# Performance work log

Measured on AMD Instinct MI355X. Metric: run time of the kernel, lower is better.

Reference implementation:

```python
import jax, jax.numpy as jnp
import numpy as np

H = 64          # hidden_size / SINDy latent dim
DM = 128        # d_model (GRU input size)
FF = 128        # dim_feedforward
NL = 2          # num_sindy_layers
EPS = 1e-5      # LayerNorm eps (torch default)
TRI_I, TRI_J = np.triu_indices(H)          # poly_order=2 pairs, torch loop order (i<=j)
LIB = 1 + H + TRI_I.size                   # 2145


def layernorm(x, g, b):
    m = jnp.mean(x, axis=-1, keepdims=True)
    v = jnp.mean((x - m) ** 2, axis=-1, keepdims=True)
    return (x - m) * jax.lax.rsqrt(v + EPS) * g + b


def sindy_library(z):
    # z: (N, H) -> Theta: (N, 1 + H + H*(H+1)/2); same term ordering as torch loops
    ones = jnp.ones((z.shape[0], 1), z.dtype)
    quad = z[:, TRI_I] * z[:, TRI_J]
    return jnp.concatenate([ones, z, quad], axis=1)


def gru_layer(x, Wih, Whh, bih, bhh):
    # x: (B, S, in), Wih: (3H, in), Whh: (3H, H); torch GRU gate order r,z,n
    xp = jnp.einsum('bsi,gi->bsg', x, Wih) + bih  # (B,S,3H) precomputed input projections
    B = x.shape[0]

    def step(h, xpt):
        gh = h @ Whh.T + bhh
        r = jax.nn.sigmoid(xpt[:, :H] + gh[:, :H])
        z = jax.nn.sigmoid(xpt[:, H:2 * H] + gh[:, H:2 * H])
        n = jnp.tanh(xpt[:, 2 * H:] + r * gh[:, 2 * H:])
        h = (1.0 - z) * n + z * h
        return h, h

    h0 = jnp.zeros((B, H), x.dtype)
    _, ys = jax.lax.scan(step, h0, jnp.swapaxes(xp, 0, 1))  # scan over time
    return jnp.swapaxes(ys, 0, 1)  # (B, S, H)


def sindy_layer(src, coef, g1, b1n, W1, bf1, W2, bf2, g2, b2n):
    B, S, _ = src.shape
    theta = sindy_library(src.reshape(-1, H))          # (N, LIB)
    upd = (theta @ coef).reshape(B, S, H)              # (B, S, H)
    src = layernorm(src + upd, g1, b1n)                # dropout = identity (eval)
    ff = jax.nn.gelu(src @ W1.T + bf1, approximate=False) @ W2.T + bf2
    return layernorm(src + ff, g2, b2n)


def setup_inputs() -> dict:
    key = jax.random.key(0)
    ks = jax.random.split(key, 24)
    f = lambda k, sh, s=0.05: (jax.random.normal(k, sh, dtype=jnp.float32) * s)
    inp = {
        'x': jax.random.normal(ks[0], (32, 500, DM), dtype=jnp.float32),
        # GRU layer 0 (input DM) and layer 1 (input H)
        'Wih0': f(ks[1], (3 * H, DM)), 'Whh0': f(ks[2], (3 * H, H)),
        'bih0': f(ks[3], (3 * H,)), 'bhh0': f(ks[4], (3 * H,)),
        'Wih1': f(ks[5], (3 * H, H)), 'Whh1': f(ks[6], (3 * H, H)),
        'bih1': f(ks[7], (3 * H,)), 'bhh1': f(ks[8], (3 * H,)),
        # stacked params for NL=2 identical SINDy layers
        'coeffs': f(ks[9], (NL, LIB, H), 0.02),
        'ln1_g': jnp.ones((NL, H), jnp.float32), 'ln1_b': jnp.zeros((NL, H), jnp.float32),
        'W1': f(ks[10], (NL, FF, H)), 'b1': f(ks[11], (NL, FF)),
        'W2': f(ks[12], (NL, H, FF)), 'b2': f(ks[13], (NL, H)),
        'ln2_g': jnp.ones((NL, H), jnp.float32), 'ln2_b': jnp.zeros((NL, H), jnp.float32),
    }
    return inp


def reference(x, Wih0, Whh0, bih0, bhh0, Wih1, Whh1, bih1, bhh1,
              coeffs, ln1_g, ln1_b, W1, b1, W2, b2, ln2_g, ln2_b):
    h = gru_layer(x, Wih0, Whh0, bih0, bhh0)
    h = gru_layer(h, Wih1, Whh1, bih1, bhh1)
    for l in range(NL):
        h = sindy_layer(h, coeffs[l], ln1_g[l], ln1_b[l], W1[l], b1[l],
                        W2[l], b2[l], ln2_g[l], ln2_b[l])
    return h, h[:, -1, :]
```

## Files before the change

### kernel.cpp

```cpp
#include <hip/hip_runtime.h>
#include <hip/hip_bf16.h>
#include <math.h>

#define H 64
#define DM 128
#define GDIM 192
#define BSZ 32
#define SEQ 500
#define NROW (BSZ*SEQ)
#define LIBN 2145
#define FFD 128
#define NKC2 75
#define NGRP 300
#define CPK2 153600

typedef __attribute__((ext_vector_type(8))) short short8;
typedef __attribute__((ext_vector_type(4))) float f32x4;
typedef __attribute__((ext_vector_type(2))) float f32x2;
typedef __attribute__((ext_vector_type(4))) unsigned u32x4;

__device__ __forceinline__ float sigf(float x) {
    return 1.0f / (1.0f + __expf(-x));
}
__device__ __forceinline__ float tanhfast(float x) {
    x = fminf(fmaxf(x, -15.0f), 15.0f);
    float t = __expf(-2.0f * x);
    return (1.0f - t) / (1.0f + t);
}
__device__ __forceinline__ short bf16r(float f) {
    unsigned u = __float_as_uint(f);
    unsigned r = (u + 0x7fffu + ((u >> 16) & 1u)) >> 16;
    return (short)r;
}
__device__ __forceinline__ f32x2 pkfma(f32x2 a, f32x2 b, f32x2 c) {
    f32x2 d;
    asm("v_pk_fma_f32 %0, %1, %2, %3" : "=v"(d) : "v"(a), "v"(b), "v"(c));
    return d;
}

__device__ __forceinline__ void grp_decode(int g, int& a, int& b) {
    if (g < 8) { a = 64; b = g * 8; }
    else if (g == 8 || g >= 297) { a = 64; b = 64; }
    else {
        int G = g - 9, acc = 0;
        a = 0; b = 0;
        for (int i2 = 0; i2 < 64; i2++) {
            int cnt = 8 - (i2 >> 3);
            if (G < acc + cnt) { a = i2; b = ((i2 >> 3) + (G - acc)) * 8; break; }
            acc += cnt;
        }
    }
}

__global__ void pack_all(const float* __restrict__ wih0,
                         const float* __restrict__ coeffs,
                         const float* __restrict__ w1,
                         const float* __restrict__ w2,
                         float* __restrict__ wtp,
                         short* __restrict__ bfa) {
    int idx = blockIdx.x * 256 + threadIdx.x;
    if (idx < GDIM * DM) {
        int k = idx / GDIM;
        int g = idx - k * GDIM;
        wtp[idx] = wih0[g * DM + k];
        return;
    }
    int r = idx - GDIM * DM;
    int l = r / (CPK2 + 2 * 8192);
    int q = r % (CPK2 + 2 * 8192);
    if (q < CPK2) {
        const float* coef = coeffs + (size_t)l * LIBN * H;
        int j = q & 7, lane = (q >> 3) & 63, nt = (q >> 9) & 3, kc = q >> 11;
        int grp = kc * 4 + (lane >> 4);
        int row = -1;
        if (grp < 8) row = 1 + grp * 8 + j;
        else if (grp == 8) row = (j == 0) ? 0 : -1;
        else if (grp < 297) {
            int a, b;
            grp_decode(grp, a, b);
            int jdx = b + j;
            if (jdx >= a) row = 65 + a * 64 - (a * (a - 1)) / 2 + (jdx - a);
        }
        int c = nt * 16 + (lane & 15);
        bfa[(size_t)l * CPK2 + q] = (row >= 0) ? bf16r(coef[(size_t)row * H + c]) : (short)0;
        return;
    }
    int q2 = q - CPK2;
    if (q2 < 8192) {
        const float* w1l = w1 + (size_t)l * FFD * H;
        int j = q2 & 7, lane = (q2 >> 3) & 63, nt = (q2 >> 9) & 7, kc = q2 >> 12;
        int k = kc * 32 + ((lane >> 4) << 3) + j;
        int n = nt * 16 + (lane & 15);
        bfa[(size_t)2 * CPK2 + l * 8192 + q2] = bf16r(w1l[(size_t)n * H + k]);
        return;
    }
    int q3 = q2 - 8192;
    const float* w2l = w2 + (size_t)l * H * FFD;
    int j = q3 & 7, lane = (q3 >> 3) & 63, nt = (q3 >> 9) & 3, kc = q3 >> 11;
    int k = kc * 32 + ((lane >> 4) << 3) + j;
    int n = nt * 16 + (lane & 15);
    bfa[(size_t)2 * CPK2 + 2 * 8192 + l * 8192 + q3] = bf16r(w2l[(size_t)n * FFD + k]);
}

__global__ __launch_bounds__(256, 1) void xp0_gemm(const float* __restrict__ x,
                                                   const float* __restrict__ wt2,
                                                   const float* __restrict__ bih0,
                                                   float* __restrict__ xpT) {
    __shared__ __align__(16) float wlds[DM * GDIM];
    int tid = threadIdx.x;
    int wv = __builtin_amdgcn_readfirstlane(tid >> 6);
    int lane = tid & 63;

    for (int p = tid; p < DM * GDIM / 4; p += 256)
        ((f32x4*)wlds)[p] = ((const f32x4*)wt2)[p];

    int i = lane >> 2;
    int j = lane & 3;
    int rb = blockIdx.x * 64;
    int row0 = rb + 4 * i;

    f32x4 acc[3][4];
#pragma unroll
    for (int t = 0; t < 3; t++) {
        f32x4 bv = *(const f32x4*)(bih0 + 16 * (wv + 4 * t) + 4 * j);
#pragma unroll
        for (int ii = 0; ii < 4; ii++) acc[t][ii] = bv;
    }
    __syncthreads();

    const float* xr0 = x + (size_t)row0 * DM;
    for (int k4 = 0; k4 < 32; k4++) {
        f32x4 xr[4];
#pragma unroll
        for (int ii = 0; ii < 4; ii++)
            xr[ii] = *(const f32x4*)(xr0 + ii * DM + k4 * 4);
#pragma unroll
        for (int t = 0; t < 3; t++) {
            int cb = 16 * (wv + 4 * t);
#pragma unroll
            for (int e = 0; e < 4; e++) {
                f32x4 wvv = *(const f32x4*)&wlds[(k4 * 4 + e) * GDIM + cb + 4 * j];
#pragma unroll
                for (int ii = 0; ii < 4; ii++)
                    acc[t][ii] += wvv * xr[ii][e];
            }
        }
    }
    int bb = row0 / 500;
    int ss = row0 - bb * 500;
    float* base = xpT + ((size_t)(bb * 125 + (ss >> 2)) * GDIM) * 4;
#pragma unroll
    for (int t = 0; t < 3; t++) {
        int cb = 16 * (wv + 4 * t);
#pragma unroll
        for (int jj = 0; jj < 4; jj++) {
            int g = cb + 4 * j + jj;
            f32x4 v = { acc[t][0][jj], acc[t][1][jj], acc[t][2][jj], acc[t][3][jj] };
            *(f32x4*)(base + (size_t)g * 4) = v;
        }
    }
}

__global__ __launch_bounds__(768, 3) void gru_fused(const float* __restrict__ xpT,
                                                    const float* __restrict__ whh0,
                                                    const float* __restrict__ bhh0,
                                                    const float* __restrict__ wih1,
                                                    const float* __restrict__ bih1,
                                                    const float* __restrict__ whh1,
                                                    const float* __restrict__ bhh1,
                                                    float* __restrict__ hbuf) {
    int b = blockIdx.x;
    int tid = threadIdx.x;
    int wv = __builtin_amdgcn_readfirstlane(tid >> 6);
    int lane = tid & 63;
    int m = wv % 3;
    int q = wv / 3;
    int k0 = q * 16;

    __shared__ __align__(16) float h0s[H];
    __shared__ __align__(16) float h1s[H];
    __shared__ float part[3][4][GDIM];

    if (tid < H) { h0s[tid] = 0.0f; h1s[tid] = 0.0f; }

    const float* W = (m == 0) ? whh0 : (m == 1) ? wih1 : whh1;
    f32x2 wrp[8], wzp[8], wnp[8];
#pragma unroll
    for (int k4 = 0; k4 < 4; k4++) {
        f32x4 a = ((const f32x4*)(W + (size_t)lane * H + k0))[k4];
        f32x4 c = ((const f32x4*)(W + (size_t)(H + lane) * H + k0))[k4];
        f32x4 d = ((const f32x4*)(W + (size_t)(2 * H + lane) * H + k0))[k4];
        wrp[2*k4]   = __builtin_shufflevector(a, a, 0, 1);
        wrp[2*k4+1] = __builtin_shufflevector(a, a, 2, 3);
        wzp[2*k4]   = __builtin_shufflevector(c, c, 0, 1);
        wzp[2*k4+1] = __builtin_shufflevector(c, c, 2, 3);
        wnp[2*k4]   = __builtin_shufflevector(d, d, 0, 1);
        wnp[2*k4+1] = __builtin_shufflevector(d, d, 2, 3);
    }

    float b0r = 0, b0z = 0, b0n = 0;
    float b1ir = 0, b1iz = 0, b1in = 0, b1hr = 0, b1hz = 0, b1hn = 0;
    float hreg0 = 0.0f, hreg1 = 0.0f;
    float hb4[4] = {0.f, 0.f, 0.f, 0.f};
    f32x4 xc[4][3];
    const float* xpB = xpT + (size_t)b * 125 * GDIM * 4;

    if (wv == 0) {
        b0r = bhh0[lane]; b0z = bhh0[H + lane]; b0n = bhh0[2 * H + lane];
#pragma unroll
        for (int g3 = 0; g3 < 3; g3++) {
            xc[0][g3] = *(const f32x4*)(xpB + ((size_t)0 * GDIM + g3 * 64 + lane) * 4);
            xc[1][g3] = *(const f32x4*)(xpB + ((size_t)1 * GDIM + g3 * 64 + lane) * 4);
        }
    } else if (wv == 2) {
        b1ir = bih1[lane]; b1iz = bih1[H + lane]; b1in = bih1[2 * H + lane];
        b1hr = bhh1[lane]; b1hz = bhh1[H + lane]; b1hn = bhh1[2 * H + lane];
    }
    __syncthreads();

    auto loadch = [&](int c, int buf) {
        if (c < 125) {
#pragma unroll
            for (int g3 = 0; g3 < 3; g3++)
                xc[buf][g3] = *(const f32x4*)(xpB + ((size_t)c * GDIM + g3 * 64 + lane) * 4);
        }
    };

    auto step = [&](int s, int e, float xr, float xz, float xn) {
        const float* hv = (m == 2) ? h1s : h0s;
        f32x2 arp = {0.f, 0.f}, azp = {0.f, 0.f}, anp = {0.f, 0.f};
#pragma unroll
        for (int t4 = 0; t4 < 4; t4++) {
            f32x4 h4 = ((const f32x4*)(hv + k0))[t4];
            f32x2 hlo = __builtin_shufflevector(h4, h4, 0, 1);
            f32x2 hhi = __builtin_shufflevector(h4, h4, 2, 3);
            arp = pkfma(wrp[2*t4], hlo, arp);
            arp = pkfma(wrp[2*t4+1], hhi, arp);
            azp = pkfma(wzp[2*t4], hlo, azp);
            azp = pkfma(wzp[2*t4+1], hhi, azp);
            anp = pkfma(wnp[2*t4], hlo, anp);
            anp = pkfma(wnp[2*t4+1], hhi, anp);
        }
        part[m][q][lane] = arp[0] + arp[1];
        part[m][q][H + lane] = azp[0] + azp[1];
        part[m][q][2 * H + lane] = anp[0] + anp[1];
        __syncthreads();

        if (wv == 0) {
            if (s < SEQ) {
                float gr = b0r, gz = b0z, gn = b0n;
#pragma unroll
                for (int qq = 0; qq < 4; qq++) {
                    gr += part[0][qq][lane];
                    gz += part[0][qq][H + lane];
                    gn += part[0][qq][2 * H + lane];
                }
                float rg = sigf(xr + gr);
                float zg = sigf(xz + gz);
                float ng = tanhfast(xn + rg * gn);
                hreg0 = (1.0f - zg) * ng + zg * hreg0;
                h0s[lane] = hreg0;
            }
        } else if (wv == 2) {
            if (s >= 1) {
                float xr1 = b1ir, xz1 = b1iz, xn1 = b1in;
                float gr1 = b1hr, gz1 = b1hz, gn1 = b1hn;
#pragma unroll
                for (int qq = 0; qq < 4; qq++) {
                    xr1 += part[1][qq][lane];
                    xz1 += part[1][qq][H + lane];
                    xn1 += part[1][qq][2 * H + lane];
                    gr1 += part[2][qq][lane];
                    gz1 += part[2][qq][H + lane];
                    gn1 += part[2][qq][2 * H + lane];
                }
                float rg = sigf(xr1 + gr1);
                float zg = sigf(xz1 + gz1);
                float ng = tanhfast(xn1 + rg * gn1);
                hreg1 = (1.0f - zg) * ng + zg * hreg1;
                h1s[lane] = hreg1;
                hb4[(e + 3) & 3] = hreg1;
                if (e == 0) {
                    float* dst = hbuf + ((size_t)b * SEQ + (s - 4)) * H + lane;
#pragma unroll
                    for (int t = 0; t < 4; t++) dst[t * H] = hb4[t];
                }
            }
        }
        __syncthreads();
    };

    for (int scb = 0; scb < 31; scb++) {
#pragma unroll
        for (int sci = 0; sci < 4; sci++) {
            int sc = scb * 4 + sci;
            if (wv == 0 && (sci & 1) == 0) {
                loadch(sc + 2, (sci + 2) & 3);
                loadch(sc + 3, (sci + 3) & 3);
            }
            int s0 = sc * 4;
            step(s0 + 0, 0, xc[sci][0][0], xc[sci][1][0], xc[sci][2][0]);
            step(s0 + 1, 1, xc[sci][0][1], xc[sci][1][1], xc[sci][2][1]);
            step(s0 + 2, 2, xc[sci][0][2], xc[sci][1][2], xc[sci][2][2]);
            step(s0 + 3, 3, xc[sci][0][3], xc[sci][1][3], xc[sci][2][3]);
        }
    }
    {
        step(496, 0, xc[0][0][0], xc[0][1][0], xc[0][2][0]);
        step(497, 1, xc[0][0][1], xc[0][1][1], xc[0][2][1]);
        step(498, 2, xc[0][0][2], xc[0][1][2], xc[0][2][2]);
        step(499, 3, xc[0][0][3], xc[0][1][3], xc[0][2][3]);
    }
    step(500, 0, 0.0f, 0.0f, 0.0f);
}

__global__ __launch_bounds__(512) void sindy_fused(const float* __restrict__ hbuf_in,
                                                   const short* __restrict__ bfa,
                                                   const float* __restrict__ ln1g,
                                                   const float* __restrict__ ln1b,
                                                   const float* __restrict__ b1g,
                                                   const float* __restrict__ b2g,
                                                   const float* __restrict__ ln2g,
                                                   const float* __restrict__ ln2b,
                                                   float* __restrict__ out) {
    __shared__ float z[65 * 68];
    __shared__ float upd[64 * 68];
    __shared__ float ff[64 * 132];
    __shared__ unsigned kmap2[NGRP];
    __shared__ float bfs1[2][FFD], bfs2[2][H];
    __shared__ float g1s[2][H], b1s[2][H], g2s[2][H], b2s[2][H];

    int tid = threadIdx.x;
    int wv = __builtin_amdgcn_readfirstlane(tid >> 6);
    int lane = tid & 63;
    int row0 = blockIdx.x * 64;

    for (int idx = tid; idx < 64 * 16; idx += 512) {
        int r = idx >> 4, c4 = idx & 15;
        *(f32x4*)&z[r * 68 + c4 * 4] = *(const f32x4*)&hbuf_in[(size_t)(row0 + r) * H + c4 * 4];
    }
    for (int idx = tid; idx < 64 * 17; idx += 512)
        *(f32x4*)&upd[idx * 4] = (f32x4){0.f, 0.f, 0.f, 0.f};
    if (tid < 64) {
        z[tid * 68 + 64] = 1.0f; z[tid * 68 + 65] = 0.0f;
        z[tid * 68 + 66] = 0.0f; z[tid * 68 + 67] = 0.0f;
    }
    if (tid < 68) z[64 * 68 + tid] = 0.0f;
    if (tid < NGRP) {
        int a, b;
        grp_decode(tid, a, b);
        kmap2[tid] = ((unsigned)a << 16) | (unsigned)b;
    }
    if (tid < FFD) { bfs1[0][tid] = b1g[tid]; bfs1[1][tid] = b1g[FFD + tid]; }
    if (tid < H) {
        bfs2[0][tid] = b2g[tid];      bfs2[1][tid] = b2g[H + tid];
        g1s[0][tid] = ln1g[tid];      g1s[1][tid] = ln1g[H + tid];
        b1s[0][tid] = ln1b[tid];      b1s[1][tid] = ln1b[H + tid];
        g2s[0][tid] = ln2g[tid];      g2s[1][tid] = ln2g[H + tid];
        b2s[0][tid] = ln2b[tid];      b2s[1][tid] = ln2b[H + tid];
    }
    __syncthreads();

    int kj0 = ((lane >> 4) << 3);
    int m0 = (wv & 3) * 16;
    int m = m0 + (lane & 15);
    int rbase = m0 + ((lane >> 4) << 2);
    int cb16 = lane & 15;
    const float* zrow = &z[m * 68];
    int lrow = tid >> 3;
    int lk = (tid & 7) * 8;

#pragma unroll
    for (int l = 0; l < 2; l++) {
        const short* cpk = bfa + (size_t)l * CPK2;
        const short* w1p = bfa + (size_t)2 * CPK2 + l * 8192;
        const short* w2p = bfa + (size_t)2 * CPK2 + 2 * 8192 + l * 8192;

        {
            int p = wv >> 2;
            f32x4 acc[4] = {{0,0,0,0},{0,0,0,0},{0,0,0,0},{0,0,0,0}};
            for (int kc = p; kc < NKC2; kc += 2) {
                unsigned ab = kmap2[kc * 4 + (lane >> 4)];
                float za = zrow[ab >> 16];
                const float* zb = &zrow[ab & 0xffffu];
                f32x4 z0 = *(const f32x4*)zb;
                f32x4 z1 = *(const f32x4*)(zb + 4);
                short8 af;
                af[0] = bf16r(za * z0[0]);
                af[1] = bf16r(za * z0[1]);
                af[2] = bf16r(za * z0[2]);
                af[3] = bf16r(za * z0[3]);
                af[4] = bf16r(za * z1[0]);
                af[5] = bf16r(za * z1[1]);
                af[6] = bf16r(za * z1[2]);
                af[7] = bf16r(za * z1[3]);
                const short* cb = cpk + ((size_t)(kc * 4) * 64 + lane) * 8;
#pragma unroll
                for (int nt = 0; nt < 4; nt++) {
                    short8 bf = *(const short8*)(cb + (size_t)nt * 512);
                    acc[nt] = __builtin_amdgcn_mfma_f32_16x16x32_bf16(af, bf, acc[nt], 0, 0, 0);
                }
            }
#pragma unroll
            for (int nt = 0; nt < 4; nt++)
#pragma unroll
                for (int r = 0; r < 4; r++)
                    atomicAdd(&upd[(rbase + r) * 68 + nt * 16 + cb16], acc[nt][r]);
        }
        __syncthreads();

        {
            float v[8];
            float s1 = 0.0f;
#pragma unroll
            for (int i = 0; i < 8; i++) {
                v[i] = z[lrow * 68 + lk + i] + upd[lrow * 68 + lk + i];
                s1 += v[i];
            }
            s1 += __shfl_xor(s1, 1); s1 += __shfl_xor(s1, 2); s1 += __shfl_xor(s1, 4);
            float mn = s1 * (1.0f / 64.0f);
            float s2 = 0.0f;
#pragma unroll
            for (int i = 0; i < 8; i++) { float d = v[i] - mn; s2 += d * d; }
            s2 += __shfl_xor(s2, 1); s2 += __shfl_xor(s2, 2); s2 += __shfl_xor(s2, 4);
            float rstd = 1.0f / sqrtf(s2 * (1.0f / 64.0f) + 1e-5f);
#pragma unroll
            for (int i = 0; i < 8; i++)
                z[lrow * 68 + lk + i] = (v[i] - mn) * rstd * g1s[l][lk + i] + b1s[l][lk + i];
        }
        __syncthreads();

        {
            int nq = wv >> 2;
            f32x4 acc[4] = {{0,0,0,0},{0,0,0,0},{0,0,0,0},{0,0,0,0}};
#pragma unroll
            for (int kc = 0; kc < 2; kc++) {
                f32x4 za = *(const f32x4*)&z[m * 68 + kc * 32 + kj0];
                f32x4 zb = *(const f32x4*)&z[m * 68 + kc * 32 + kj0 + 4];
                short8 af;
                af[0] = bf16r(za[0]); af[1] = bf16r(za[1]); af[2] = bf16r(za[2]); af[3] = bf16r(za[3]);
                af[4] = bf16r(zb[0]); af[5] = bf16r(zb[1]); af[6] = bf16r(zb[2]); af[7] = bf16r(zb[3]);
#pragma unroll
                for (int t = 0; t < 4; t++) {
                    int nt = nq * 4 + t;
                    short8 bf = *(const short8*)(w1p + ((size_t)(kc * 8 + nt) * 64 + lane) * 8);
                    acc[t] = __builtin_amdgcn_mfma_f32_16x16x32_bf16(af, bf, acc[t], 0, 0, 0);
                }
            }
#pragma unroll
            for (int t = 0; t < 4; t++) {
                int col = (nq * 4 + t) * 16 + cb16;
#pragma unroll
                for (int r = 0; r < 4; r++) {
                    float v = acc[t][r] + bfs1[l][col];
                    ff[(rbase + r) * 132 + col] = 0.5f * v * (1.0f + erff(v * 0.70710678118654752f));
                }
            }
        }
        __syncthreads();

        {
            int nh = wv >> 2;
            f32x4 acc[2] = {{0,0,0,0},{0,0,0,0}};
            const float* frow = &ff[m * 132];
#pragma unroll
            for (int kc = 0; kc < 4; kc++) {
                f32x4 fa = *(const f32x4*)&frow[kc * 32 + kj0];
                f32x4 fb = *(const f32x4*)&frow[kc * 32 + kj0 + 4];
                short8 af;
                af[0] = bf16r(fa[0]); af[1] = bf16r(fa[1]); af[2] = bf16r(fa[2]); af[3] = bf16r(fa[3]);
                af[4] = bf16r(fb[0]); af[5] = bf16r(fb[1]); af[6] = bf16r(fb[2]); af[7] = bf16r(fb[3]);
#pragma unroll
                for (int t = 0; t < 2; t++) {
                    int nt = nh * 2 + t;
                    short8 bf = *(const short8*)(w2p + ((size_t)(kc * 4 + nt) * 64 + lane) * 8);
                    acc[t] = __builtin_amdgcn_mfma_f32_16x16x32_bf16(af, bf, acc[t], 0, 0, 0);
                }
            }
#pragma unroll
            for (int t = 0; t < 2; t++) {
                int col = (nh * 2 + t) * 16 + cb16;
#pragma unroll
                for (int r = 0; r < 4; r++)
                    upd[(rbase + r) * 68 + col] = acc[t][r] + bfs2[l][col];
            }
        }
        __syncthreads();

        {
            float v[8];
            float s1 = 0.0f;
#pragma unroll
            for (int i = 0; i < 8; i++) {
                v[i] = z[lrow * 68 + lk + i] + upd[lrow * 68 + lk + i];
                s1 += v[i];
            }
            s1 += __shfl_xor(s1, 1); s1 += __shfl_xor(s1, 2); s1 += __shfl_xor(s1, 4);
            float mn = s1 * (1.0f / 64.0f);
            float s2 = 0.0f;
#pragma unroll
            for (int i = 0; i < 8; i++) { float d = v[i] - mn; s2 += d * d; }
            s2 += __shfl_xor(s2, 1); s2 += __shfl_xor(s2, 2); s2 += __shfl_xor(s2, 4);
            float rstd = 1.0f / sqrtf(s2 * (1.0f / 64.0f) + 1e-5f);
            if (l == 0) {
#pragma unroll
                for (int i = 0; i < 8; i++)
                    z[lrow * 68 + lk + i] = (v[i] - mn) * rstd * g2s[0][lk + i] + b2s[0][lk + i];
            } else {
                int row = row0 + lrow;
                int last = (row % SEQ == SEQ - 1);
#pragma unroll
                for (int i = 0; i < 8; i++) {
                    float res = (v[i] - mn) * rstd * g2s[1][lk + i] + b2s[1][lk + i];
                    out[(size_t)row * H + lk + i] = res;
                    if (last)
                        out[(size_t)NROW * H + (row / SEQ) * H + lk + i] = res;
                }
            }
        }
        __syncthreads();

        if (l == 0) {
            for (int idx = tid; idx < 64 * 17; idx += 512)
                *(f32x4*)&upd[idx * 4] = (f32x4){0.f, 0.f, 0.f, 0.f};
            __syncthreads();
        }
    }
}

extern "C" void kernel_launch(void* const* d_in, const int* in_sizes, int n_in,
                              void* d_out, int out_size, void* d_ws, size_t ws_size,
                              hipStream_t stream) {
    const float* x    = (const float*)d_in[0];
    const float* wih0 = (const float*)d_in[1];
    const float* whh0 = (const float*)d_in[2];
    const float* bih0 = (const float*)d_in[3];
    const float* bhh0 = (const float*)d_in[4];
    const float* wih1 = (const float*)d_in[5];
    const float* whh1 = (const float*)d_in[6];
    const float* bih1 = (const float*)d_in[7];
    const float* bhh1 = (const float*)d_in[8];
    const float* coeffs = (const float*)d_in[9];
    const float* ln1g = (const float*)d_in[10];
    const float* ln1b = (const float*)d_in[11];
    const float* w1   = (const float*)d_in[12];
    const float* b1   = (const float*)d_in[13];
    const float* w2   = (const float*)d_in[14];
    const float* b2   = (const float*)d_in[15];
    const float* ln2g = (const float*)d_in[16];
    const float* ln2b = (const float*)d_in[17];

    float* out = (float*)d_out;
    float* ws  = (float*)d_ws;
    float* xpT = ws;
    float* wtp = ws + (size_t)NROW * GDIM;
    short* bfa = (short*)(wtp + GDIM * DM);
    float* hbuf = out;

    pack_all<<<1424, 256, 0, stream>>>(wih0, coeffs, w1, w2, wtp, bfa);
    xp0_gemm<<<NROW / 64, 256, 0, stream>>>(x, wtp, bih0, xpT);
    gru_fused<<<BSZ, 768, 0, stream>>>(xpT, whh0, bhh0, wih1, bih1, whh1, bhh1, hbuf);
    sindy_fused<<<NROW / 64, 512, 0, stream>>>(hbuf, bfa, ln1g, ln1b, b1, b2,
                                               ln2g, ln2b, out);
}
```

Measured before the change: 465.8 us.

## Replicate GRU gate math across all waves to use one barrier per step

Restructures the fused two-layer GRU recurrence so every wave computes the gate nonlinearities redundantly for its own slice, reading partial sums from double-buffered shared memory and reducing them with lane shuffles. The hidden state is then broadcast within each wave by shuffles instead of through shared h vectors. This cuts the per-timestep synchronization from two barriers to one lightweight waitcnt+barrier and removes the serial dependence on a single wave doing the gate math. In exchange every wave issues its own input-projection loads and does redundant transcendental work, and the raw s_barrier asm relies on the double buffering being correct.

```diff
diff --git a/kernel.cpp b/kernel.cpp
--- a/kernel.cpp
+++ b/kernel.cpp
@@ -13,6 +13,7 @@
 #define NKC2 75
 #define NGRP 300
 #define CPK2 153600
+#define PSTR 196
 
 typedef __attribute__((ext_vector_type(8))) short short8;
 typedef __attribute__((ext_vector_type(4))) float f32x4;
@@ -37,6 +38,8 @@
     asm("v_pk_fma_f32 %0, %1, %2, %3" : "=v"(d) : "v"(a), "v"(b), "v"(c));
     return d;
 }
+
+#define BAR_LGKM() asm volatile("s_waitcnt lgkmcnt(0)\n\ts_barrier" ::: "memory")
 
 __device__ __forceinline__ void grp_decode(int g, int& a, int& b) {
     if (g < 8) { a = 64; b = g * 8; }
@@ -176,12 +179,13 @@
     int m = wv % 3;
     int q = wv / 3;
     int k0 = q * 16;
-
-    __shared__ __align__(16) float h0s[H];
-    __shared__ __align__(16) float h1s[H];
-    __shared__ float part[3][4][GDIM];
-
-    if (tid < H) { h0s[tid] = 0.0f; h1s[tid] = 0.0f; }
+    int kel = k0 + (lane >> 2);
+    int qq = lane & 3;
+
+    __shared__ float part[2][3][4][PSTR];
+
+    for (int i = tid; i < 2 * 3 * 4 * PSTR; i += 768)
+        ((float*)part)[i] = 0.0f;
 
     const float* W = (m == 0) ? whh0 : (m == 1) ? wih1 : whh1;
     f32x2 wrp[8], wzp[8], wnp[8];
@@ -198,120 +202,119 @@
         wnp[2*k4+1] = __builtin_shufflevector(d, d, 2, 3);
     }
 
-    float b0r = 0, b0z = 0, b0n = 0;
-    float b1ir = 0, b1iz = 0, b1in = 0, b1hr = 0, b1hz = 0, b1hn = 0;
-    float hreg0 = 0.0f, hreg1 = 0.0f;
-    float hb4[4] = {0.f, 0.f, 0.f, 0.f};
-    f32x4 xc[4][3];
+    float br, bz, bn, cr = 0.f, cz = 0.f, cn = 0.f;
+    if (m <= 1) {
+        br = bhh0[kel]; bz = bhh0[H + kel]; bn = bhh0[2 * H + kel];
+    } else {
+        br = bih1[kel]; bz = bih1[H + kel]; bn = bih1[2 * H + kel];
+        cr = bhh1[kel]; cz = bhh1[H + kel]; cn = bhh1[2 * H + kel];
+    }
+
+    float hprev = 0.0f;
+    float hbv = 0.0f;
+    f32x4 xq[4][3];
+#pragma unroll
+    for (int s = 0; s < 4; s++)
+#pragma unroll
+        for (int g = 0; g < 3; g++) xq[s][g] = (f32x4){0.f, 0.f, 0.f, 0.f};
     const float* xpB = xpT + (size_t)b * 125 * GDIM * 4;
 
-    if (wv == 0) {
-        b0r = bhh0[lane]; b0z = bhh0[H + lane]; b0n = bhh0[2 * H + lane];
-#pragma unroll
-        for (int g3 = 0; g3 < 3; g3++) {
-            xc[0][g3] = *(const f32x4*)(xpB + ((size_t)0 * GDIM + g3 * 64 + lane) * 4);
-            xc[1][g3] = *(const f32x4*)(xpB + ((size_t)1 * GDIM + g3 * 64 + lane) * 4);
-        }
-    } else if (wv == 2) {
-        b1ir = bih1[lane]; b1iz = bih1[H + lane]; b1in = bih1[2 * H + lane];
-        b1hr = bhh1[lane]; b1hz = bhh1[H + lane]; b1hn = bhh1[2 * H + lane];
-    }
+    auto pre = [&](int c, int slot) {
+        if (m <= 1 && c < 125) {
+            xq[slot][0] = *(const f32x4*)(xpB + ((size_t)c * GDIM + kel) * 4);
+            xq[slot][1] = *(const f32x4*)(xpB + ((size_t)c * GDIM + 64 + kel) * 4);
+            xq[slot][2] = *(const f32x4*)(xpB + ((size_t)c * GDIM + 128 + kel) * 4);
+        }
+    };
+    pre(0, 0);
+    pre(1, 1);
     __syncthreads();
 
-    auto loadch = [&](int c, int buf) {
-        if (c < 125) {
-#pragma unroll
-            for (int g3 = 0; g3 < 3; g3++)
-                xc[buf][g3] = *(const f32x4*)(xpB + ((size_t)c * GDIM + g3 * 64 + lane) * 4);
-        }
-    };
-
-    auto step = [&](int s, int e, float xr, float xz, float xn) {
-        const float* hv = (m == 2) ? h1s : h0s;
-        f32x2 arp = {0.f, 0.f}, azp = {0.f, 0.f}, anp = {0.f, 0.f};
-#pragma unroll
-        for (int t4 = 0; t4 < 4; t4++) {
-            f32x4 h4 = ((const f32x4*)(hv + k0))[t4];
-            f32x2 hlo = __builtin_shufflevector(h4, h4, 0, 1);
-            f32x2 hhi = __builtin_shufflevector(h4, h4, 2, 3);
-            arp = pkfma(wrp[2*t4], hlo, arp);
-            arp = pkfma(wrp[2*t4+1], hhi, arp);
-            azp = pkfma(wzp[2*t4], hlo, azp);
-            azp = pkfma(wzp[2*t4+1], hhi, azp);
-            anp = pkfma(wnp[2*t4], hlo, anp);
-            anp = pkfma(wnp[2*t4+1], hhi, anp);
-        }
-        part[m][q][lane] = arp[0] + arp[1];
-        part[m][q][H + lane] = azp[0] + azp[1];
-        part[m][q][2 * H + lane] = anp[0] + anp[1];
-        __syncthreads();
-
-        if (wv == 0) {
-            if (s < SEQ) {
-                float gr = b0r, gz = b0z, gn = b0n;
-#pragma unroll
-                for (int qq = 0; qq < 4; qq++) {
-                    gr += part[0][qq][lane];
-                    gz += part[0][qq][H + lane];
-                    gn += part[0][qq][2 * H + lane];
-                }
-                float rg = sigf(xr + gr);
-                float zg = sigf(xz + gz);
-                float ng = tanhfast(xn + rg * gn);
-                hreg0 = (1.0f - zg) * ng + zg * hreg0;
-                h0s[lane] = hreg0;
-            }
-        } else if (wv == 2) {
-            if (s >= 1) {
-                float xr1 = b1ir, xz1 = b1iz, xn1 = b1in;
-                float gr1 = b1hr, gz1 = b1hz, gn1 = b1hn;
-#pragma unroll
-                for (int qq = 0; qq < 4; qq++) {
-                    xr1 += part[1][qq][lane];
-                    xz1 += part[1][qq][H + lane];
-                    xn1 += part[1][qq][2 * H + lane];
-                    gr1 += part[2][qq][lane];
-                    gz1 += part[2][qq][H + lane];
-                    gn1 += part[2][qq][2 * H + lane];
-                }
-                float rg = sigf(xr1 + gr1);
-                float zg = sigf(xz1 + gz1);
-                float ng = tanhfast(xn1 + rg * gn1);
-                hreg1 = (1.0f - zg) * ng + zg * hreg1;
-                h1s[lane] = hreg1;
-                hb4[(e + 3) & 3] = hreg1;
-                if (e == 0) {
-                    float* dst = hbuf + ((size_t)b * SEQ + (s - 4)) * H + lane;
-#pragma unroll
-                    for (int t = 0; t < 4; t++) dst[t * H] = hb4[t];
-                }
-            }
-        }
-        __syncthreads();
+    auto step = [&](int u, int e, int slot) {
+        BAR_LGKM();
+        int rd = (e + 1) & 1;
+        float hnew = hprev;
+        if (m <= 1) {
+            if (u < SEQ) {
+                float pr = part[rd][0][qq][kel];
+                float pz = part[rd][0][qq][H + kel];
+                float pn = part[rd][0][qq][2 * H + kel];
+                pr += __shfl_xor(pr, 1); pr += __shfl_xor(pr, 2);
+                pz += __shfl_xor(pz, 1); pz += __shfl_xor(pz, 2);
+                pn += __shfl_xor(pn, 1); pn += __shfl_xor(pn, 2);
+                float rg = sigf(xq[slot][0][e] + pr + br);
+                float zg = sigf(xq[slot][1][e] + pz + bz);
+                float ng = tanhfast(xq[slot][2][e] + rg * (pn + bn));
+                hnew = (1.0f - zg) * ng + zg * hprev;
+                hprev = hnew;
+            }
+        } else {
+            if (u >= 1) {
+                float ar = part[rd][1][qq][kel];
+                float az = part[rd][1][qq][H + kel];
+                float an = part[rd][1][qq][2 * H + kel];
+                float gr = part[rd][2][qq][kel];
+                float gz = part[rd][2][qq][H + kel];
+                float gn = part[rd][2][qq][2 * H + kel];
+                ar += __shfl_xor(ar, 1); ar += __shfl_xor(ar, 2);
+                az += __shfl_xor(az, 1); az += __shfl_xor(az, 2);
+                an += __shfl_xor(an, 1); an += __shfl_xor(an, 2);
+                gr += __shfl_xor(gr, 1); gr += __shfl_xor(gr, 2);
+                gz += __shfl_xor(gz, 1); gz += __shfl_xor(gz, 2);
+                gn += __shfl_xor(gn, 1); gn += __shfl_xor(gn, 2);
+                float rg = sigf((ar + br) + (gr + cr));
+                float zg = sigf((az + bz) + (gz + cz));
+                float ng = tanhfast((an + bn) + rg * (gn + cn));
+                hnew = (1.0f - zg) * ng + zg * hprev;
+                hprev = hnew;
+                if (((e + 3) & 3) == qq) hbv = hnew;
+                if (e == 0 && u >= 4)
+                    hbuf[((size_t)b * SEQ + (u - 4) + qq) * H + kel] = hbv;
+            }
+        }
+        if (m == 2 || u < SEQ) {
+            f32x2 hp[8];
+#pragma unroll
+            for (int t = 0; t < 8; t++) {
+                hp[t][0] = __shfl(hnew, 8 * t);
+                hp[t][1] = __shfl(hnew, 8 * t + 4);
+            }
+            f32x2 arp = {0.f, 0.f}, azp = {0.f, 0.f}, anp = {0.f, 0.f};
+#pragma unroll
+            for (int t = 0; t < 8; t++) {
+                arp = pkfma(wrp[t], hp[t], arp);
+                azp = pkfma(wzp[t], hp[t], azp);
+                anp = pkfma(wnp[t], hp[t], anp);
+            }
+            int wb = e & 1;
+            part[wb][m][q][lane]         = arp[0] + arp[1];
+            part[wb][m][q][H + lane]     = azp[0] + azp[1];
+            part[wb][m][q][2 * H + lane] = anp[0] + anp[1];
+        }
     };
 
     for (int scb = 0; scb < 31; scb++) {
 #pragma unroll
         for (int sci = 0; sci < 4; sci++) {
             int sc = scb * 4 + sci;
-            if (wv == 0 && (sci & 1) == 0) {
-                loadch(sc + 2, (sci + 2) & 3);
-                loadch(sc + 3, (sci + 3) & 3);
+            if ((sci & 1) == 0) {
+                pre(sc + 2, (sci + 2) & 3);
+                pre(sc + 3, (sci + 3) & 3);
             }
             int s0 = sc * 4;
-            step(s0 + 0, 0, xc[sci][0][0], xc[sci][1][0], xc[sci][2][0]);
-            step(s0 + 1, 1, xc[sci][0][1], xc[sci][1][1], xc[sci][2][1]);
-            step(s0 + 2, 2, xc[sci][0][2], xc[sci][1][2], xc[sci][2][2]);
-            step(s0 + 3, 3, xc[sci][0][3], xc[sci][1][3], xc[sci][2][3]);
+            step(s0 + 0, 0, sci);
+            step(s0 + 1, 1, sci);
+            step(s0 + 2, 2, sci);
+            step(s0 + 3, 3, sci);
         }
     }
     {
-        step(496, 0, xc[0][0][0], xc[0][1][0], xc[0][2][0]);
-        step(497, 1, xc[0][0][1], xc[0][1][1], xc[0][2][1]);
-        step(498, 2, xc[0][0][2], xc[0][1][2], xc[0][2][2]);
-        step(499, 3, xc[0][0][3], xc[0][1][3], xc[0][2][3]);
-    }
-    step(500, 0, 0.0f, 0.0f, 0.0f);
+        step(496, 0, 0);
+        step(497, 1, 0);
+        step(498, 2, 0);
+        step(499, 3, 0);
+    }
+    step(500, 0, 0);
 }
 
 __global__ __launch_bounds__(512) void sindy_fused(const float* __restrict__ hbuf_in,
```

Result: slower. 793.9 us (+70.4%).

## Pack two batch sequences per GRU block with 2-way K split

Applied to the files above, without the earlier changes.

The fused GRU kernel now runs two batch sequences per 768-thread block, each using 6 waves with a 2-way K split (32 columns per wave) instead of 4-way. This halves the grid and the number of partial sums reduced per step, but doubles the weight registers per wave and the per-wave dot-product length on the serial recurrence critical path. The shared barriers now couple the two sequences.

```diff
diff --git a/kernel.cpp b/kernel.cpp
--- a/kernel.cpp
+++ b/kernel.cpp
@@ -169,24 +169,26 @@
                                                     const float* __restrict__ whh1,
                                                     const float* __restrict__ bhh1,
                                                     float* __restrict__ hbuf) {
-    int b = blockIdx.x;
     int tid = threadIdx.x;
     int wv = __builtin_amdgcn_readfirstlane(tid >> 6);
     int lane = tid & 63;
-    int m = wv % 3;
-    int q = wv / 3;
-    int k0 = q * 16;
-
-    __shared__ __align__(16) float h0s[H];
-    __shared__ __align__(16) float h1s[H];
-    __shared__ float part[3][4][GDIM];
-
-    if (tid < H) { h0s[tid] = 0.0f; h1s[tid] = 0.0f; }
+    int sq = wv / 6;
+    int wl = wv % 6;
+    int m = wl >> 1;
+    int q = wl & 1;
+    int k0 = q * 32;
+    int b = blockIdx.x * 2 + sq;
+
+    __shared__ __align__(16) float h0s[2][H];
+    __shared__ __align__(16) float h1s[2][H];
+    __shared__ float part[2][3][2][GDIM];
+
+    if (tid < 2 * H) { ((float*)h0s)[tid] = 0.0f; ((float*)h1s)[tid] = 0.0f; }
 
     const float* W = (m == 0) ? whh0 : (m == 1) ? wih1 : whh1;
-    f32x2 wrp[8], wzp[8], wnp[8];
-#pragma unroll
-    for (int k4 = 0; k4 < 4; k4++) {
+    f32x2 wrp[16], wzp[16], wnp[16];
+#pragma unroll
+    for (int k4 = 0; k4 < 8; k4++) {
         f32x4 a = ((const f32x4*)(W + (size_t)lane * H + k0))[k4];
         f32x4 c = ((const f32x4*)(W + (size_t)(H + lane) * H + k0))[k4];
         f32x4 d = ((const f32x4*)(W + (size_t)(2 * H + lane) * H + k0))[k4];
@@ -205,14 +207,14 @@
     f32x4 xc[4][3];
     const float* xpB = xpT + (size_t)b * 125 * GDIM * 4;
 
-    if (wv == 0) {
+    if (wl == 0) {
         b0r = bhh0[lane]; b0z = bhh0[H + lane]; b0n = bhh0[2 * H + lane];
 #pragma unroll
         for (int g3 = 0; g3 < 3; g3++) {
             xc[0][g3] = *(const f32x4*)(xpB + ((size_t)0 * GDIM + g3 * 64 + lane) * 4);
             xc[1][g3] = *(const f32x4*)(xpB + ((size_t)1 * GDIM + g3 * 64 + lane) * 4);
         }
-    } else if (wv == 2) {
+    } else if (wl == 4) {
         b1ir = bih1[lane]; b1iz = bih1[H + lane]; b1in = bih1[2 * H + lane];
         b1hr = bhh1[lane]; b1hz = bhh1[H + lane]; b1hn = bhh1[2 * H + lane];
     }
@@ -227,10 +229,10 @@
     };
 
     auto step = [&](int s, int e, float xr, float xz, float xn) {
-        const float* hv = (m == 2) ? h1s : h0s;
+        const float* hv = (m == 2) ? h1s[sq] : h0s[sq];
         f32x2 arp = {0.f, 0.f}, azp = {0.f, 0.f}, anp = {0.f, 0.f};
 #pragma unroll
-        for (int t4 = 0; t4 < 4; t4++) {
+        for (int t4 = 0; t4 < 8; t4++) {
             f32x4 h4 = ((const f32x4*)(hv + k0))[t4];
             f32x2 hlo = __builtin_shufflevector(h4, h4, 0, 1);
             f32x2 hhi = __builtin_shufflevector(h4, h4, 2, 3);
@@ -241,44 +243,35 @@
             anp = pkfma(wnp[2*t4], hlo, anp);
             anp = pkfma(wnp[2*t4+1], hhi, anp);
         }
-        part[m][q][lane] = arp[0] + arp[1];
-        part[m][q][H + lane] = azp[0] + azp[1];
-        part[m][q][2 * H + lane] = anp[0] + anp[1];
-        __syncthreads();
-
-        if (wv == 0) {
+        part[sq][m][q][lane]         = arp[0] + arp[1];
+        part[sq][m][q][H + lane]     = azp[0] + azp[1];
+        part[sq][m][q][2 * H + lane] = anp[0] + anp[1];
+        __syncthreads();
+
+        if (wl == 0) {
             if (s < SEQ) {
-                float gr = b0r, gz = b0z, gn = b0n;
-#pragma unroll
-                for (int qq = 0; qq < 4; qq++) {
-                    gr += part[0][qq][lane];
-                    gz += part[0][qq][H + lane];
-                    gn += part[0][qq][2 * H + lane];
-                }
+                float gr = b0r + part[sq][0][0][lane] + part[sq][0][1][lane];
+                float gz = b0z + part[sq][0][0][H + lane] + part[sq][0][1][H + lane];
+                float gn = b0n + part[sq][0][0][2*H + lane] + part[sq][0][1][2*H + lane];
                 float rg = sigf(xr + gr);
                 float zg = sigf(xz + gz);
                 float ng = tanhfast(xn + rg * gn);
                 hreg0 = (1.0f - zg) * ng + zg * hreg0;
-                h0s[lane] = hreg0;
-            }
-        } else if (wv == 2) {
+                h0s[sq][lane] = hreg0;
+            }
+        } else if (wl == 4) {
             if (s >= 1) {
-                float xr1 = b1ir, xz1 = b1iz, xn1 = b1in;
-                float gr1 = b1hr, gz1 = b1hz, gn1 = b1hn;
-#pragma unroll
-                for (int qq = 0; qq < 4; qq++) {
-                    xr1 += part[1][qq][lane];
-                    xz1 += part[1][qq][H + lane];
-                    xn1 += part[1][qq][2 * H + lane];
-                    gr1 += part[2][qq][lane];
-                    gz1 += part[2][qq][H + lane];
-                    gn1 += part[2][qq][2 * H + lane];
-                }
+                float xr1 = b1ir + part[sq][1][0][lane] + part[sq][1][1][lane];
+                float xz1 = b1iz + part[sq][1][0][H + lane] + part[sq][1][1][H + lane];
+                float xn1 = b1in + part[sq][1][0][2*H + lane] + part[sq][1][1][2*H + lane];
+                float gr1 = b1hr + part[sq][2][0][lane] + part[sq][2][1][lane];
+                float gz1 = b1hz + part[sq][2][0][H + lane] + part[sq][2][1][H + lane];
+                float gn1 = b1hn + part[sq][2][0][2*H + lane] + part[sq][2][1][2*H + lane];
                 float rg = sigf(xr1 + gr1);
                 float zg = sigf(xz1 + gz1);
                 float ng = tanhfast(xn1 + rg * gn1);
                 hreg1 = (1.0f - zg) * ng + zg * hreg1;
-                h1s[lane] = hreg1;
+                h1s[sq][lane] = hreg1;
                 hb4[(e + 3) & 3] = hreg1;
                 if (e == 0) {
                     float* dst = hbuf + ((size_t)b * SEQ + (s - 4)) * H + lane;
@@ -294,7 +287,7 @@
 #pragma unroll
         for (int sci = 0; sci < 4; sci++) {
             int sc = scb * 4 + sci;
-            if (wv == 0 && (sci & 1) == 0) {
+            if (wl == 0 && (sci & 1) == 0) {
                 loadch(sc + 2, (sci + 2) & 3);
                 loadch(sc + 3, (sci + 3) & 3);
             }
@@ -559,7 +552,7 @@
 
     pack_all<<<1424, 256, 0, stream>>>(wih0, coeffs, w1, w2, wtp, bfa);
     xp0_gemm<<<NROW / 64, 256, 0, stream>>>(x, wtp, bih0, xpT);
-    gru_fused<<<BSZ, 768, 0, stream>>>(xpT, whh0, bhh0, wih1, bih1, whh1, bhh1, hbuf);
+    gru_fused<<<BSZ / 2, 768, 0, stream>>>(xpT, whh0, bhh0, wih1, bih1, whh1, bhh1, hbuf);
     sindy_fused<<<NROW / 64, 512, 0, stream>>>(hbuf, bfa, ln1g, ln1b, b1, b2,
                                                ln2g, ln2b, out);
 }
```

Measured after the change: 672.4 us. 44.3% more time.
